# Performance work log

Hardware: AMD Instinct MI355X
Metric: run time of the kernel (lower is better)

The kernel has to match this reference:

```python
import jax, jax.numpy as jnp
import numpy as np

GRID = (32, 32, 32)  # must match init grid_size


def setup_inputs() -> dict:
    key = jax.random.key(0)
    # Mimic the module's init: D = 0.01 everywhere + 0.1 on the 6x6 diagonal,
    # plus small uniform noise so the baseline exercises non-degenerate values.
    D = jax.random.uniform(key, (6, 6, *GRID), dtype=jnp.float32) * 0.02 + 0.01
    D = D.at[jnp.arange(6), jnp.arange(6)].add(0.1)
    return {"D": D, "sx": 1, "sy": 1, "sz": 1, "ex": 30, "ey": 30, "ez": 30,
            "max_iterations": 300}


def reference(D, sx, sy, sz, ex, ey, ez, max_iterations):
    """flash_wave (training path, inference=False): 300-step CA as one lax.scan.

    Returns the stacked history of phi (pre-update, as the torch loop appends
    phi at the top of each iteration): shape [max_iterations, 6, X, Y, Z].
    Early exit is emulated by freezing phi once the wave reaches (ex,ey,ez),
    so no per-step host sync is needed.
    """
    phi0 = jnp.zeros((6, *GRID), dtype=D.dtype).at[:, sx, sy, sz].set(1.0)
    active_D = D + 0.95  # inference=False branch

    def body(carry, _):
        phi, done = carry
        # 6x6 channel mixing per grid cell: 'oixyz,ixyz->oxyz'
        phi_out = jnp.einsum('oixyz,ixyz->oxyz', active_D, phi)
        pn = jnp.zeros_like(phi)
        pn = pn.at[0, 1:, :, :].set(phi_out[0, :-1, :, :])   # +x
        pn = pn.at[1, :-1, :, :].set(phi_out[1, 1:, :, :])   # -x
        pn = pn.at[2, :, 1:, :].set(phi_out[2, :, :-1, :])   # +y
        pn = pn.at[3, :, :-1, :].set(phi_out[3, :, 1:, :])   # -y
        pn = pn.at[4, :, :, 1:].set(phi_out[4, :, :, :-1])   # +z
        pn = pn.at[5, :, :, :-1].set(phi_out[5, :, :, 1:])   # -z
        nxt = jnp.clip(pn, 0.0, 1.0)
        nxt = jnp.where(done, phi, nxt)  # freeze after target reached
        reached = jnp.sum(nxt[:, ex, ey, ez]) > 0.01
        return (nxt, jnp.logical_or(done, reached)), phi

    (_, _), history = jax.lax.scan(body, (phi0, jnp.array(False)), None,
                                   length=int(max_iterations))
    return history
```

## Files before the change

kernel.cpp:

```cpp
#include <hip/hip_runtime.h>

#define NCH 6
#define NX 32
#define PLANE 1024
#define NCELL (NX * PLANE)
#define STEP_STRIDE (NCH * NCELL)
#define NTHREADS 256
#define NBLOCKS 128
#define RB 2

#define RING_WORDS ((size_t)RB * 3 * NCELL)
#define F_DONE 0

typedef unsigned long long u64;

__device__ __forceinline__ u64 ld64(const u64* p) {
    return __hip_atomic_load(p, __ATOMIC_RELAXED, __HIP_MEMORY_SCOPE_SYSTEM);
}
__device__ __forceinline__ void st64(u64* p, u64 v) {
    __hip_atomic_store(p, v, __ATOMIC_RELAXED, __HIP_MEMORY_SCOPE_SYSTEM);
}
__device__ __forceinline__ int ldi(const int* p) {
    return __hip_atomic_load(p, __ATOMIC_RELAXED, __HIP_MEMORY_SCOPE_SYSTEM);
}
__device__ __forceinline__ void sti(int* p, int v) {
    __hip_atomic_store(p, v, __ATOMIC_RELAXED, __HIP_MEMORY_SCOPE_SYSTEM);
}
__device__ __forceinline__ u64 pack2p(float a, float b, unsigned P) {
    const u64 w = ((u64)__float_as_uint(b) << 32) | __float_as_uint(a);
    return P ? (w | 0x8000000080000000ULL) : w;
}
__device__ __forceinline__ bool tagok(u64 w, unsigned P) {
    return (((unsigned)(w >> 63)) == P) & ((((unsigned)w) >> 31) == P);
}
__device__ __forceinline__ void unpack2(u64 w, float* d0, float* d1) {
    *d0 = __uint_as_float((unsigned)w & 0x7fffffffu);
    *d1 = __uint_as_float((unsigned)(w >> 32) & 0x7fffffffu);
}

__global__ void __launch_bounds__(NTHREADS)
BEMNA_V7_2_PhaseSpace_44117904064519_kernel(
    const float* __restrict__ D,
    const int* __restrict__ sx_p, const int* __restrict__ sy_p,
    const int* __restrict__ sz_p, const int* __restrict__ ex_p,
    const int* __restrict__ ey_p, const int* __restrict__ ez_p,
    const int* __restrict__ maxit_p,
    float* __restrict__ out,
    u64* __restrict__ ring,
    int* __restrict__ flags)
{
    const int tid  = (int)threadIdx.x;
    const int cell = (int)blockIdx.x * NTHREADS + tid;
    const int lane = tid & 63;
    const int x = cell >> 10;
    const int y = (cell >> 5) & 31;
    const int z = cell & 31;

    const int sx = *sx_p, sy = *sy_p, sz = *sz_p;
    const int ex = *ex_p, ey = *ey_p, ez = *ez_p;
    const int maxit = *maxit_p;
    const bool is_seed   = (cell == ((sx << 10) | (sy << 5) | sz));
    const bool is_target = (cell == ((ex << 10) | (ey << 5) | ez));

    const int  nbg[NCH] = { cell - PLANE, cell + PLANE, cell - 32, cell + 32, cell - 1, cell + 1 };
    const bool ok[NCH]  = { x >= 1, x <= 30, y >= 1, y <= 30, z >= 1, z <= 30 };

    const int cxm = ok[0] ? cell - PLANE : cell;
    const int cxp = ok[1] ? cell + PLANE : cell;
    const bool hi = (lane >= 32);
    const int cye = hi ? (ok[3] ? cell + 32 : cell)
                       : (ok[2] ? cell - 32 : cell);

    float dreg[NCH][NCH];
#pragma unroll
    for (int o = 0; o < NCH; ++o)
#pragma unroll
        for (int i = 0; i < NCH; ++i)
            dreg[o][i] = ok[o] ? D[(size_t)(o * NCH + i) * NCELL + nbg[o]] + 0.95f : 0.0f;

    float myv[NCH];
    const float iv = is_seed ? 1.0f : 0.0f;
    {
        const u64 p = pack2p(iv, iv, 0);
        st64(&ring[0 * NCELL + cell], p);
        st64(&ring[1 * NCELL + cell], p);
        st64(&ring[2 * NCELL + cell], p);
        float* outp = out + cell;
#pragma unroll
        for (int o = 0; o < NCH; ++o) { myv[o] = iv; outp[o * NCELL] = iv; }
    }

    int tripped = 0;
    for (int t = 0; t <= maxit - 2; ++t) {
        const u64* r0 = ring + (size_t)(t & 1) * 3 * NCELL;
        const u64* r1 = r0 + NCELL;
        const u64* r2 = r1 + NCELL;
        const unsigned P = (unsigned)((t >> 1) & 1);

        u64 a0, a1, a2, b0, b1, b2, c0, c1, c2;
        int ab = 0;
        for (;;) {
            a0 = ld64(r0 + cxm); a1 = ld64(r1 + cxm); a2 = ld64(r2 + cxm);
            b0 = ld64(r0 + cxp); b1 = ld64(r1 + cxp); b2 = ld64(r2 + cxp);
            c0 = ld64(r0 + cye); c1 = ld64(r1 + cye); c2 = ld64(r2 + cye);
            int dn = -1;
            if (lane == 0) dn = ldi(&flags[F_DONE]);
            dn = __shfl(dn, 0);
            const bool okr = tagok(a0, P) & tagok(a1, P) & tagok(a2, P)
                           & tagok(b0, P) & tagok(b1, P) & tagok(b2, P)
                           & tagok(c0, P) & tagok(c1, P) & tagok(c2, P);
            if (dn >= 0 && t + 1 > dn) { ab = 1; break; }
            if (__ballot(okr) == ~0ull) break;
            __builtin_amdgcn_s_sleep(1);
        }
        if (ab) break;

        float xm[NCH], xp[NCH], ye[NCH];
        unpack2(a0, &xm[0], &xm[1]); unpack2(a1, &xm[2], &xm[3]); unpack2(a2, &xm[4], &xm[5]);
        unpack2(b0, &xp[0], &xp[1]); unpack2(b1, &xp[2], &xp[3]); unpack2(b2, &xp[4], &xp[5]);
        unpack2(c0, &ye[0], &ye[1]); unpack2(c1, &ye[2], &ye[3]); unpack2(c2, &ye[4], &ye[5]);

        float ym[NCH], yp[NCH], zm[NCH], zp[NCH];
#pragma unroll
        for (int i = 0; i < NCH; ++i) {
            const float yin = __shfl(myv[i], lane ^ 32);
            zm[i] = __shfl(myv[i], (lane - 1) & 63);
            zp[i] = __shfl(myv[i], (lane + 1) & 63);
            ym[i] = hi ? yin : ye[i];
            yp[i] = hi ? ye[i] : yin;
        }

        float v[NCH];
        {
            float s0 = 0.f, s1 = 0.f, s2 = 0.f, s3 = 0.f, s4 = 0.f, s5 = 0.f;
#pragma unroll
            for (int i = 0; i < NCH; ++i) {
                s0 = fmaf(dreg[0][i], xm[i], s0);
                s1 = fmaf(dreg[1][i], xp[i], s1);
                s2 = fmaf(dreg[2][i], ym[i], s2);
                s3 = fmaf(dreg[3][i], yp[i], s3);
                s4 = fmaf(dreg[4][i], zm[i], s4);
                s5 = fmaf(dreg[5][i], zp[i], s5);
            }
            v[0] = fminf(fmaxf(s0, 0.f), 1.f);
            v[1] = fminf(fmaxf(s1, 0.f), 1.f);
            v[2] = fminf(fmaxf(s2, 0.f), 1.f);
            v[3] = fminf(fmaxf(s3, 0.f), 1.f);
            v[4] = fminf(fmaxf(s4, 0.f), 1.f);
            v[5] = fminf(fmaxf(s5, 0.f), 1.f);
        }

        if (is_target && !tripped) {
            if (v[0] + v[1] + v[2] + v[3] + v[4] + v[5] > 0.01f) {
                sti(&flags[F_DONE], t + 1);
                tripped = 1;
            }
        }

        {
            const unsigned P1 = (unsigned)(((t + 1) >> 1) & 1);
            u64* w0 = ring + (size_t)((t + 1) & 1) * 3 * NCELL;
            st64(w0 + 0 * NCELL + cell, pack2p(v[0], v[1], P1));
            st64(w0 + 1 * NCELL + cell, pack2p(v[2], v[3], P1));
            st64(w0 + 2 * NCELL + cell, pack2p(v[4], v[5], P1));
        }

        {
            float* outp = out + (size_t)(t + 1) * STEP_STRIDE + cell;
#pragma unroll
            for (int o = 0; o < NCH; ++o) outp[o * NCELL] = v[o];
        }
#pragma unroll
        for (int o = 0; o < NCH; ++o) myv[o] = v[o];
    }
}

__global__ void fill_kernel(const int* __restrict__ flags,
                            float4* __restrict__ out,
                            int total4)
{
    const int s4 = STEP_STRIDE / 4;
    const int maxit = total4 / s4;
    const int ds = flags[F_DONE];
    const int tf = (ds >= 1 && ds <= maxit - 1) ? ds : maxit - 1;
    const int idx = (int)blockIdx.x * (int)blockDim.x + (int)threadIdx.x;
    const float4 v = out[(size_t)tf * s4 + idx];
    for (int t = tf + 1; t < maxit; ++t)
        out[(size_t)t * s4 + idx] = v;
}

extern "C" void kernel_launch(void* const* d_in, const int* in_sizes, int n_in,
                              void* d_out, int out_size, void* d_ws, size_t ws_size,
                              hipStream_t stream)
{
    const float* D   = (const float*)d_in[0];
    const int* sx    = (const int*)d_in[1];
    const int* sy    = (const int*)d_in[2];
    const int* sz    = (const int*)d_in[3];
    const int* ex    = (const int*)d_in[4];
    const int* ey    = (const int*)d_in[5];
    const int* ez    = (const int*)d_in[6];
    const int* maxit = (const int*)d_in[7];
    float* out = (float*)d_out;

    u64* ring  = (u64*)d_ws;
    int* flags = (int*)(ring + RING_WORDS);

    BEMNA_V7_2_PhaseSpace_44117904064519_kernel<<<dim3(NBLOCKS), dim3(NTHREADS), 0, stream>>>(
        D, sx, sy, sz, ex, ey, ez, maxit, out, ring, flags);

    const int total4 = out_size / 4;
    fill_kernel<<<dim3((STEP_STRIDE / 4) / 256), dim3(256), 0, stream>>>(
        flags, (float4*)out, total4);
}
```

Before: 406.6 us.

## Fuse two CA steps per grid sync using halo-expanded LDS tiles

Each block now owns a 1x8x32 slab and loads a halo-extended 3x12x32 tile from the global ring into shared memory. It computes an intermediate step over a 3x10 region redundantly, then the owned step from it. This halves the number of cross-block global ring handshakes per simulated step, which is the dominant latency, in exchange for redundant compute, larger blocks of 1024 threads and more LDS traffic. The fill kernel also gains a second grid dimension so the tail copy of the frozen state is split across more blocks.

```diff
diff --git a/kernel.cpp b/kernel.cpp
--- a/kernel.cpp
+++ b/kernel.cpp
@@ -5,9 +5,11 @@
 #define PLANE 1024
 #define NCELL (NX * PLANE)
 #define STEP_STRIDE (NCH * NCELL)
-#define NTHREADS 256
+#define NTHREADS 1024
 #define NBLOCKS 128
 #define RB 2
+#define NE 960
+#define NT3 1152
 
 #define RING_WORDS ((size_t)RB * 3 * NCELL)
 #define F_DONE 0
@@ -38,7 +40,7 @@
     *d1 = __uint_as_float((unsigned)(w >> 32) & 0x7fffffffu);
 }
 
-__global__ void __launch_bounds__(NTHREADS)
+__global__ void __launch_bounds__(NTHREADS, 1)
 BEMNA_V7_2_PhaseSpace_44117904064519_kernel(
     const float* __restrict__ D,
     const int* __restrict__ sx_p, const int* __restrict__ sy_p,
@@ -49,129 +51,202 @@
     u64* __restrict__ ring,
     int* __restrict__ flags)
 {
-    const int tid  = (int)threadIdx.x;
-    const int cell = (int)blockIdx.x * NTHREADS + tid;
-    const int lane = tid & 63;
-    const int x = cell >> 10;
-    const int y = (cell >> 5) & 31;
-    const int z = cell & 31;
+    __shared__ float Tb[NCH][NT3];
+    __shared__ float Eb[NCH][NE];
+    __shared__ int lds_dn;
+    volatile int* vdn = &lds_dn;
+
+    const int tid = (int)threadIdx.x;
+    const int bx  = (int)blockIdx.x;
+    const int x   = bx >> 2;
+    const int ys  = (bx & 3) << 3;
 
     const int sx = *sx_p, sy = *sy_p, sz = *sz_p;
-    const int ex = *ex_p, ey = *ey_p, ez = *ez_p;
+    const int ex = *ex_p, ey = *ey_p, ez_ = *ez_p;
     const int maxit = *maxit_p;
-    const bool is_seed   = (cell == ((sx << 10) | (sy << 5) | sz));
-    const bool is_target = (cell == ((ex << 10) | (ey << 5) | ez));
-
-    const int  nbg[NCH] = { cell - PLANE, cell + PLANE, cell - 32, cell + 32, cell - 1, cell + 1 };
-    const bool ok[NCH]  = { x >= 1, x <= 30, y >= 1, y <= 30, z >= 1, z <= 30 };
-
-    const int cxm = ok[0] ? cell - PLANE : cell;
-    const int cxp = ok[1] ? cell + PLANE : cell;
-    const bool hi = (lane >= 32);
-    const int cye = hi ? (ok[3] ? cell + 32 : cell)
-                       : (ok[2] ? cell - 32 : cell);
-
+    const int seedc = (sx << 10) | (sy << 5) | sz;
+    const int targc = (ex << 10) | (ey << 5) | ez_;
+
+    const int anchor = (x << 10) + (ys << 5) + (tid & 31);
+
+    int cTA = anchor, slA = 0; bool inA = false;
+    if (tid < NT3) {
+        const int dp = tid / 384, rem = tid - dp * 384;
+        const int r2 = rem >> 5, zz = rem & 31;
+        const int gx = x - 1 + dp, gy = ys - 2 + r2;
+        slA = tid;
+        if (gx >= 0 && gx < 32 && gy >= 0 && gy < 32) { inA = true; cTA = (gx << 10) + (gy << 5) + zz; }
+    }
+    int cTB = anchor, slB = 0; bool inB = false;
+    if (tid < NT3 - 1024) {
+        const int slot = tid + 1024;
+        const int dp = slot / 384, rem = slot - dp * 384;
+        const int r2 = rem >> 5, zz = rem & 31;
+        const int gx = x - 1 + dp, gy = ys - 2 + r2;
+        slB = slot;
+        if (gx >= 0 && gx < 32 && gy >= 0 && gy < 32) { inB = true; cTB = (gx << 10) + (gy << 5) + zz; }
+    }
+
+    const bool eact = (tid < NE);
+    int dx = 0, ry = 0, ez = tid & 31, xe = x, ye = ys;
+    bool ein = false;
+    int celle = anchor;
+    if (eact) {
+        dx = tid / 320; const int rem = tid - dx * 320; ry = rem >> 5; ez = rem & 31;
+        xe = x - 1 + dx; ye = ys - 1 + ry;
+        ein = (xe >= 0 && xe < 32 && ye >= 0 && ye < 32);
+        if (ein) celle = (xe << 10) + (ye << 5) + ez;
+    }
+    const bool own = ein && (dx == 1) && (ry >= 1) && (ry <= 8);
+    const bool is_seed   = own && (celle == seedc);
+    const bool is_target = own && (celle == targc);
+
+    int cP = anchor;
+    if (eact && ein && dx == 0 && x - 2 >= 0)  cP = ((x - 2) << 10) + (ye << 5) + ez;
+    if (eact && ein && dx == 2 && x + 2 <= 31) cP = ((x + 2) << 10) + (ye << 5) + ez;
+
+    const int  nbg[NCH] = { celle - PLANE, celle + PLANE, celle - 32, celle + 32, celle - 1, celle + 1 };
+    const bool okn[NCH] = { ein && xe >= 1, ein && xe <= 30, ein && ye >= 1,
+                            ein && ye <= 30, ein && ez >= 1, ein && ez <= 30 };
     float dreg[NCH][NCH];
 #pragma unroll
     for (int o = 0; o < NCH; ++o)
 #pragma unroll
         for (int i = 0; i < NCH; ++i)
-            dreg[o][i] = ok[o] ? D[(size_t)(o * NCH + i) * NCELL + nbg[o]] + 0.95f : 0.0f;
-
-    float myv[NCH];
-    const float iv = is_seed ? 1.0f : 0.0f;
-    {
+            dreg[o][i] = okn[o] ? D[(size_t)(o * NCH + i) * NCELL + nbg[o]] + 0.95f : 0.0f;
+
+    const int ts3  = (dx * 12 + ry + 1) * 32 + ez;
+    const int tpa0 = (ts3 - 384 >= 0) ? ts3 - 384 : 0;
+    const int tpa1 = (ts3 + 384 < NT3) ? ts3 + 384 : NT3 - 1;
+    const int tp2 = ts3 - 32, tp3 = ts3 + 32;
+    const int tp4 = (ez >= 1) ? ts3 - 1 : ts3, tp5 = (ez <= 30) ? ts3 + 1 : ts3;
+    const int en0 = tid - 320, en1 = tid + 320, en2 = tid - 32, en3 = tid + 32;
+    const int en4 = (ez >= 1) ? tid - 1 : tid, en5 = (ez <= 30) ? tid + 1 : tid;
+
+    for (int k = tid; k < NCH * NT3; k += NTHREADS) ((float*)Tb)[k] = 0.0f;
+    for (int k = tid; k < NCH * NE;  k += NTHREADS) ((float*)Eb)[k] = 0.0f;
+    if (tid == 0) lds_dn = -1;
+    if (own) {
+        const float iv = is_seed ? 1.0f : 0.0f;
         const u64 p = pack2p(iv, iv, 0);
-        st64(&ring[0 * NCELL + cell], p);
-        st64(&ring[1 * NCELL + cell], p);
-        st64(&ring[2 * NCELL + cell], p);
-        float* outp = out + cell;
-#pragma unroll
-        for (int o = 0; o < NCH; ++o) { myv[o] = iv; outp[o * NCELL] = iv; }
-    }
+        st64(&ring[0 * NCELL + celle], p);
+        st64(&ring[1 * NCELL + celle], p);
+        st64(&ring[2 * NCELL + celle], p);
+#pragma unroll
+        for (int o = 0; o < NCH; ++o) out[o * NCELL + celle] = iv;
+    }
+    __syncthreads();
 
     int tripped = 0;
-    for (int t = 0; t <= maxit - 2; ++t) {
-        const u64* r0 = ring + (size_t)(t & 1) * 3 * NCELL;
+    for (int ss = 0; 2 * ss + 1 <= maxit - 1; ++ss) {
+        const u64* r0 = ring + (size_t)(ss & 1) * 3 * NCELL;
         const u64* r1 = r0 + NCELL;
         const u64* r2 = r1 + NCELL;
-        const unsigned P = (unsigned)((t >> 1) & 1);
-
-        u64 a0, a1, a2, b0, b1, b2, c0, c1, c2;
-        int ab = 0;
+        const unsigned P = (unsigned)((ss >> 1) & 1);
+
+        u64 a0, a1, a2, b0, b1, b2, p0, p1, p2;
         for (;;) {
-            a0 = ld64(r0 + cxm); a1 = ld64(r1 + cxm); a2 = ld64(r2 + cxm);
-            b0 = ld64(r0 + cxp); b1 = ld64(r1 + cxp); b2 = ld64(r2 + cxp);
-            c0 = ld64(r0 + cye); c1 = ld64(r1 + cye); c2 = ld64(r2 + cye);
-            int dn = -1;
-            if (lane == 0) dn = ldi(&flags[F_DONE]);
-            dn = __shfl(dn, 0);
+            a0 = ld64(r0 + cTA); a1 = ld64(r1 + cTA); a2 = ld64(r2 + cTA);
+            b0 = ld64(r0 + cTB); b1 = ld64(r1 + cTB); b2 = ld64(r2 + cTB);
+            p0 = ld64(r0 + cP);  p1 = ld64(r1 + cP);  p2 = ld64(r2 + cP);
+            int dnv = -1;
+            if ((tid & 63) == 0) dnv = ldi(&flags[F_DONE]);
+            if (dnv >= 0) *vdn = dnv;
             const bool okr = tagok(a0, P) & tagok(a1, P) & tagok(a2, P)
                            & tagok(b0, P) & tagok(b1, P) & tagok(b2, P)
-                           & tagok(c0, P) & tagok(c1, P) & tagok(c2, P);
-            if (dn >= 0 && t + 1 > dn) { ab = 1; break; }
+                           & tagok(p0, P) & tagok(p1, P) & tagok(p2, P);
+            const int d = *vdn;
+            if (d >= 0 && 2 * ss + 1 > d) break;
             if (__ballot(okr) == ~0ull) break;
             __builtin_amdgcn_s_sleep(1);
         }
-        if (ab) break;
-
-        float xm[NCH], xp[NCH], ye[NCH];
-        unpack2(a0, &xm[0], &xm[1]); unpack2(a1, &xm[2], &xm[3]); unpack2(a2, &xm[4], &xm[5]);
-        unpack2(b0, &xp[0], &xp[1]); unpack2(b1, &xp[2], &xp[3]); unpack2(b2, &xp[4], &xp[5]);
-        unpack2(c0, &ye[0], &ye[1]); unpack2(c1, &ye[2], &ye[3]); unpack2(c2, &ye[4], &ye[5]);
-
-        float ym[NCH], yp[NCH], zm[NCH], zp[NCH];
-#pragma unroll
-        for (int i = 0; i < NCH; ++i) {
-            const float yin = __shfl(myv[i], lane ^ 32);
-            zm[i] = __shfl(myv[i], (lane - 1) & 63);
-            zp[i] = __shfl(myv[i], (lane + 1) & 63);
-            ym[i] = hi ? yin : ye[i];
-            yp[i] = hi ? ye[i] : yin;
-        }
-
-        float v[NCH];
-        {
+        if (inA) {
+            unpack2(a0, &Tb[0][slA], &Tb[1][slA]);
+            unpack2(a1, &Tb[2][slA], &Tb[3][slA]);
+            unpack2(a2, &Tb[4][slA], &Tb[5][slA]);
+        }
+        if (inB) {
+            unpack2(b0, &Tb[0][slB], &Tb[1][slB]);
+            unpack2(b1, &Tb[2][slB], &Tb[3][slB]);
+            unpack2(b2, &Tb[4][slB], &Tb[5][slB]);
+        }
+        float pX[NCH];
+        unpack2(p0, &pX[0], &pX[1]); unpack2(p1, &pX[2], &pX[3]); unpack2(p2, &pX[4], &pX[5]);
+
+        __syncthreads();
+        { const int d = *vdn; if (d >= 0 && 2 * ss + 1 > d) break; }
+
+        float v1[NCH] = {0, 0, 0, 0, 0, 0};
+        if (eact) {
             float s0 = 0.f, s1 = 0.f, s2 = 0.f, s3 = 0.f, s4 = 0.f, s5 = 0.f;
 #pragma unroll
             for (int i = 0; i < NCH; ++i) {
-                s0 = fmaf(dreg[0][i], xm[i], s0);
-                s1 = fmaf(dreg[1][i], xp[i], s1);
-                s2 = fmaf(dreg[2][i], ym[i], s2);
-                s3 = fmaf(dreg[3][i], yp[i], s3);
-                s4 = fmaf(dreg[4][i], zm[i], s4);
-                s5 = fmaf(dreg[5][i], zp[i], s5);
-            }
-            v[0] = fminf(fmaxf(s0, 0.f), 1.f);
-            v[1] = fminf(fmaxf(s1, 0.f), 1.f);
-            v[2] = fminf(fmaxf(s2, 0.f), 1.f);
-            v[3] = fminf(fmaxf(s3, 0.f), 1.f);
-            v[4] = fminf(fmaxf(s4, 0.f), 1.f);
-            v[5] = fminf(fmaxf(s5, 0.f), 1.f);
-        }
-
-        if (is_target && !tripped) {
-            if (v[0] + v[1] + v[2] + v[3] + v[4] + v[5] > 0.01f) {
-                sti(&flags[F_DONE], t + 1);
+                const float xi0 = (dx == 0) ? pX[i] : Tb[i][tpa0];
+                const float xi1 = (dx == 2) ? pX[i] : Tb[i][tpa1];
+                s0 = fmaf(dreg[0][i], xi0, s0);
+                s1 = fmaf(dreg[1][i], xi1, s1);
+                s2 = fmaf(dreg[2][i], Tb[i][tp2], s2);
+                s3 = fmaf(dreg[3][i], Tb[i][tp3], s3);
+                s4 = fmaf(dreg[4][i], Tb[i][tp4], s4);
+                s5 = fmaf(dreg[5][i], Tb[i][tp5], s5);
+            }
+            v1[0] = fminf(fmaxf(s0, 0.f), 1.f);
+            v1[1] = fminf(fmaxf(s1, 0.f), 1.f);
+            v1[2] = fminf(fmaxf(s2, 0.f), 1.f);
+            v1[3] = fminf(fmaxf(s3, 0.f), 1.f);
+            v1[4] = fminf(fmaxf(s4, 0.f), 1.f);
+            v1[5] = fminf(fmaxf(s5, 0.f), 1.f);
+        }
+        if (own) {
+            float* op = out + (size_t)(2 * ss + 1) * STEP_STRIDE + celle;
+#pragma unroll
+            for (int o = 0; o < NCH; ++o) op[o * NCELL] = v1[o];
+            if (is_target && !tripped &&
+                (v1[0] + v1[1] + v1[2] + v1[3] + v1[4] + v1[5] > 0.01f)) {
+                sti(&flags[F_DONE], 2 * ss + 1);
                 tripped = 1;
             }
         }
-
-        {
-            const unsigned P1 = (unsigned)(((t + 1) >> 1) & 1);
-            u64* w0 = ring + (size_t)((t + 1) & 1) * 3 * NCELL;
-            st64(w0 + 0 * NCELL + cell, pack2p(v[0], v[1], P1));
-            st64(w0 + 1 * NCELL + cell, pack2p(v[2], v[3], P1));
-            st64(w0 + 2 * NCELL + cell, pack2p(v[4], v[5], P1));
-        }
-
-        {
-            float* outp = out + (size_t)(t + 1) * STEP_STRIDE + cell;
-#pragma unroll
-            for (int o = 0; o < NCH; ++o) outp[o * NCELL] = v[o];
-        }
-#pragma unroll
-        for (int o = 0; o < NCH; ++o) myv[o] = v[o];
+        if (eact) {
+#pragma unroll
+            for (int i = 0; i < NCH; ++i) Eb[i][tid] = v1[i];
+        }
+        __syncthreads();
+
+        if (own) {
+            float s0 = 0.f, s1 = 0.f, s2 = 0.f, s3 = 0.f, s4 = 0.f, s5 = 0.f;
+#pragma unroll
+            for (int i = 0; i < NCH; ++i) {
+                s0 = fmaf(dreg[0][i], Eb[i][en0], s0);
+                s1 = fmaf(dreg[1][i], Eb[i][en1], s1);
+                s2 = fmaf(dreg[2][i], Eb[i][en2], s2);
+                s3 = fmaf(dreg[3][i], Eb[i][en3], s3);
+                s4 = fmaf(dreg[4][i], Eb[i][en4], s4);
+                s5 = fmaf(dreg[5][i], Eb[i][en5], s5);
+            }
+            float v2[NCH];
+            v2[0] = fminf(fmaxf(s0, 0.f), 1.f);
+            v2[1] = fminf(fmaxf(s1, 0.f), 1.f);
+            v2[2] = fminf(fmaxf(s2, 0.f), 1.f);
+            v2[3] = fminf(fmaxf(s3, 0.f), 1.f);
+            v2[4] = fminf(fmaxf(s4, 0.f), 1.f);
+            v2[5] = fminf(fmaxf(s5, 0.f), 1.f);
+            if (is_target && !tripped &&
+                (v2[0] + v2[1] + v2[2] + v2[3] + v2[4] + v2[5] > 0.01f)) {
+                sti(&flags[F_DONE], 2 * ss + 2);
+                tripped = 1;
+            }
+            const unsigned P1 = (unsigned)(((ss + 1) >> 1) & 1);
+            u64* w = ring + (size_t)((ss + 1) & 1) * 3 * NCELL;
+            st64(w + 0 * NCELL + celle, pack2p(v2[0], v2[1], P1));
+            st64(w + 1 * NCELL + celle, pack2p(v2[2], v2[3], P1));
+            st64(w + 2 * NCELL + celle, pack2p(v2[4], v2[5], P1));
+            if (2 * ss + 2 <= maxit - 1) {
+                float* op = out + (size_t)(2 * ss + 2) * STEP_STRIDE + celle;
+#pragma unroll
+                for (int o = 0; o < NCH; ++o) op[o * NCELL] = v2[o];
+            }
+        }
     }
 }
 
@@ -185,7 +260,7 @@
     const int tf = (ds >= 1 && ds <= maxit - 1) ? ds : maxit - 1;
     const int idx = (int)blockIdx.x * (int)blockDim.x + (int)threadIdx.x;
     const float4 v = out[(size_t)tf * s4 + idx];
-    for (int t = tf + 1; t < maxit; ++t)
+    for (int t = tf + 1 + (int)blockIdx.y; t < maxit; t += (int)gridDim.y)
         out[(size_t)t * s4 + idx] = v;
 }
 
@@ -210,6 +285,6 @@
         D, sx, sy, sz, ex, ey, ez, maxit, out, ring, flags);
 
     const int total4 = out_size / 4;
-    fill_kernel<<<dim3((STEP_STRIDE / 4) / 256), dim3(256), 0, stream>>>(
+    fill_kernel<<<dim3((STEP_STRIDE / 4) / 256, 8), dim3(256), 0, stream>>>(
         flags, (float4*)out, total4);
 }
```

New measurement: 445.1 us. +9.5%, slower.

## Tile blocks as 2x8x32 slabs with LDS halo exchange and neighbor-progress sync

Applied to the files above, without the earlier changes.

Each block now covers a 2(x) by 8(y) by 32(z) slab of cells. Neighbor values inside the block are exchanged through shared memory, so only true halo cells are polled from the global ring. Halo reads are skipped while the wavefront cannot yet have reached them, based on Manhattan distance from the seed. The ring grows to 8 slots with 2-bit tags, and blocks enforce a bounded lead over their neighbors through per-block progress flags. The fill kernel also gets a second grid dimension so the time steps after early exit are written in parallel. The aim is less global polling traffic and lower per-step sync latency, at the cost of per-step __syncthreads and more complex flag logic.

```diff
diff --git a/kernel.cpp b/kernel.cpp
--- a/kernel.cpp
+++ b/kernel.cpp
@@ -5,12 +5,14 @@
 #define PLANE 1024
 #define NCELL (NX * PLANE)
 #define STEP_STRIDE (NCH * NCELL)
-#define NTHREADS 256
-#define NBLOCKS 128
-#define RB 2
+#define NTHREADS 512
+#define NBLOCKS 64
+#define RB 8
+#define MLEAD 6
 
 #define RING_WORDS ((size_t)RB * 3 * NCELL)
 #define F_DONE 0
+#define F_PROG 16
 
 typedef unsigned long long u64;
 
@@ -26,12 +28,18 @@
 __device__ __forceinline__ void sti(int* p, int v) {
     __hip_atomic_store(p, v, __ATOMIC_RELAXED, __HIP_MEMORY_SCOPE_SYSTEM);
 }
-__device__ __forceinline__ u64 pack2p(float a, float b, unsigned P) {
-    const u64 w = ((u64)__float_as_uint(b) << 32) | __float_as_uint(a);
-    return P ? (w | 0x8000000080000000ULL) : w;
-}
-__device__ __forceinline__ bool tagok(u64 w, unsigned P) {
-    return (((unsigned)(w >> 63)) == P) & ((((unsigned)w) >> 31) == P);
+__device__ __forceinline__ u64 pack2(float a, float b) {
+    return ((u64)__float_as_uint(b) << 32) | __float_as_uint(a);
+}
+__device__ __forceinline__ u64 pack2t(float a, float b, unsigned tg) {
+    u64 w = pack2(a, b);
+    if (tg & 1u) w |= 0x80000000ULL;
+    if (tg & 2u) w |= 0x8000000000000000ULL;
+    return w;
+}
+__device__ __forceinline__ bool tagchk(u64 w, unsigned tg) {
+    return ((((unsigned)(w >> 31)) & 1u) == (tg & 1u)) &
+           ((((unsigned)(w >> 63)) & 1u) == (tg >> 1));
 }
 __device__ __forceinline__ void unpack2(u64 w, float* d0, float* d1) {
     *d0 = __uint_as_float((unsigned)w & 0x7fffffffu);
@@ -49,12 +57,21 @@
     u64* __restrict__ ring,
     int* __restrict__ flags)
 {
+    __shared__ u64 Tb[2][3][NTHREADS];
+    __shared__ int lds_dn;
+    volatile int* vdn = &lds_dn;
+
     const int tid  = (int)threadIdx.x;
-    const int cell = (int)blockIdx.x * NTHREADS + tid;
+    const int bx   = (int)blockIdx.x;
+    const int cx   = bx >> 2;
+    const int st   = bx & 3;
+    const int lx   = tid >> 8;
+    const int row  = (tid >> 5) & 7;
+    const int z    = tid & 31;
     const int lane = tid & 63;
-    const int x = cell >> 10;
-    const int y = (cell >> 5) & 31;
-    const int z = cell & 31;
+    const int gx   = (cx << 1) + lx;
+    const int gy   = (st << 3) + row;
+    const int cell = (gx << 10) + (gy << 5) + z;
 
     const int sx = *sx_p, sy = *sy_p, sz = *sz_p;
     const int ex = *ex_p, ey = *ey_p, ez = *ez_p;
@@ -62,85 +79,112 @@
     const bool is_seed   = (cell == ((sx << 10) | (sy << 5) | sz));
     const bool is_target = (cell == ((ex << 10) | (ey << 5) | ez));
 
+    const bool has_x = lx ? (gx <= 30) : (gx >= 1);
+    const int  gxh   = lx ? gx + 1 : gx - 1;
+    const int  cellx = has_x ? ((gxh << 10) + (gy << 5) + z) : cell;
+    const int  distx = abs(gxh - sx) + abs(gy - sy) + abs(z - sz);
+    const bool has_y = (row == 0) ? (gy >= 1) : ((row == 7) ? (gy <= 30) : false);
+    const int  gyh   = (row == 0) ? gy - 1 : gy + 1;
+    const int  celly = has_y ? ((gx << 10) + (gyh << 5) + z) : cell;
+    const int  disty = abs(gx - sx) + abs(gyh - sy) + abs(z - sz);
+
+    const int xin = lx ? tid - 256 : tid + 256;
+    const int yin = ((row & 1) ? tid + 32 : tid - 32) & (NTHREADS - 1);
+
     const int  nbg[NCH] = { cell - PLANE, cell + PLANE, cell - 32, cell + 32, cell - 1, cell + 1 };
-    const bool ok[NCH]  = { x >= 1, x <= 30, y >= 1, y <= 30, z >= 1, z <= 30 };
-
-    const int cxm = ok[0] ? cell - PLANE : cell;
-    const int cxp = ok[1] ? cell + PLANE : cell;
-    const bool hi = (lane >= 32);
-    const int cye = hi ? (ok[3] ? cell + 32 : cell)
-                       : (ok[2] ? cell - 32 : cell);
-
+    const bool okn[NCH] = { gx >= 1, gx <= 30, gy >= 1, gy <= 30, z >= 1, z <= 30 };
     float dreg[NCH][NCH];
 #pragma unroll
     for (int o = 0; o < NCH; ++o)
 #pragma unroll
         for (int i = 0; i < NCH; ++i)
-            dreg[o][i] = ok[o] ? D[(size_t)(o * NCH + i) * NCELL + nbg[o]] + 0.95f : 0.0f;
+            dreg[o][i] = okn[o] ? D[(size_t)(o * NCH + i) * NCELL + nbg[o]] + 0.95f : 0.0f;
 
     float myv[NCH];
     const float iv = is_seed ? 1.0f : 0.0f;
     {
-        const u64 p = pack2p(iv, iv, 0);
+        const u64 p = pack2(iv, iv);
         st64(&ring[0 * NCELL + cell], p);
         st64(&ring[1 * NCELL + cell], p);
         st64(&ring[2 * NCELL + cell], p);
-        float* outp = out + cell;
-#pragma unroll
-        for (int o = 0; o < NCH; ++o) { myv[o] = iv; outp[o * NCELL] = iv; }
+        Tb[0][0][tid] = p; Tb[0][1][tid] = p; Tb[0][2][tid] = p;
+#pragma unroll
+        for (int o = 0; o < NCH; ++o) { myv[o] = iv; out[o * NCELL + cell] = iv; }
     }
-
-    int tripped = 0;
+    if (tid == 0) { lds_dn = -1; sti(&flags[F_PROG + bx * 16], 0); }
+    __syncthreads();
+
+    int tripped = 0, lastmin = 0;
     for (int t = 0; t <= maxit - 2; ++t) {
-        const u64* r0 = ring + (size_t)(t & 1) * 3 * NCELL;
-        const u64* r1 = r0 + NCELL;
-        const u64* r2 = r1 + NCELL;
-        const unsigned P = (unsigned)((t >> 1) & 1);
-
-        u64 a0, a1, a2, b0, b1, b2, c0, c1, c2;
-        int ab = 0;
-        for (;;) {
-            a0 = ld64(r0 + cxm); a1 = ld64(r1 + cxm); a2 = ld64(r2 + cxm);
-            b0 = ld64(r0 + cxp); b1 = ld64(r1 + cxp); b2 = ld64(r2 + cxp);
-            c0 = ld64(r0 + cye); c1 = ld64(r1 + cye); c2 = ld64(r2 + cye);
-            int dn = -1;
-            if (lane == 0) dn = ldi(&flags[F_DONE]);
-            dn = __shfl(dn, 0);
-            const bool okr = tagok(a0, P) & tagok(a1, P) & tagok(a2, P)
-                           & tagok(b0, P) & tagok(b1, P) & tagok(b2, P)
-                           & tagok(c0, P) & tagok(c1, P) & tagok(c2, P);
-            if (dn >= 0 && t + 1 > dn) { ab = 1; break; }
-            if (__ballot(okr) == ~0ull) break;
-            __builtin_amdgcn_s_sleep(1);
-        }
-        if (ab) break;
-
-        float xm[NCH], xp[NCH], ye[NCH];
-        unpack2(a0, &xm[0], &xm[1]); unpack2(a1, &xm[2], &xm[3]); unpack2(a2, &xm[4], &xm[5]);
-        unpack2(b0, &xp[0], &xp[1]); unpack2(b1, &xp[2], &xp[3]); unpack2(b2, &xp[4], &xp[5]);
-        unpack2(c0, &ye[0], &ye[1]); unpack2(c1, &ye[2], &ye[3]); unpack2(c2, &ye[4], &ye[5]);
-
-        float ym[NCH], yp[NCH], zm[NCH], zp[NCH];
-#pragma unroll
-        for (int i = 0; i < NCH; ++i) {
-            const float yin = __shfl(myv[i], lane ^ 32);
-            zm[i] = __shfl(myv[i], (lane - 1) & 63);
-            zp[i] = __shfl(myv[i], (lane + 1) & 63);
-            ym[i] = hi ? yin : ye[i];
-            yp[i] = hi ? ye[i] : yin;
-        }
-
+        const u64* rs = ring + (size_t)(t & (RB - 1)) * 3 * NCELL;
+        const unsigned tg = (unsigned)((t >> 2) & 3);
+
+        const bool needx = has_x && (t >= distx);
+        const bool needy = has_y && (t >= disty);
+        float rx[NCH] = {0,0,0,0,0,0}, ry[NCH] = {0,0,0,0,0,0};
+        if (__ballot(needx || needy) != 0ull) {
+            u64 hx0 = 0, hx1 = 0, hx2 = 0, hy0 = 0, hy1 = 0, hy2 = 0;
+            for (;;) {
+                if (needx) { hx0 = ld64(rs + cellx); hx1 = ld64(rs + NCELL + cellx); hx2 = ld64(rs + 2 * NCELL + cellx); }
+                if (needy) { hy0 = ld64(rs + celly); hy1 = ld64(rs + NCELL + celly); hy2 = ld64(rs + 2 * NCELL + celly); }
+                if (lane == 0) { const int dnv = ldi(&flags[F_DONE]); if (dnv >= 0) *vdn = dnv; }
+                bool okr = true;
+                if (needx) okr = okr & tagchk(hx0, tg) & tagchk(hx1, tg) & tagchk(hx2, tg);
+                if (needy) okr = okr & tagchk(hy0, tg) & tagchk(hy1, tg) & tagchk(hy2, tg);
+                const int d = *vdn;
+                if (d >= 0 && t + 1 > d) break;
+                if (__ballot(okr) == ~0ull) break;
+                __builtin_amdgcn_s_sleep(1);
+            }
+            if (needx) { unpack2(hx0, &rx[0], &rx[1]); unpack2(hx1, &rx[2], &rx[3]); unpack2(hx2, &rx[4], &rx[5]); }
+            if (needy) { unpack2(hy0, &ry[0], &ry[1]); unpack2(hy1, &ry[2], &ry[3]); unpack2(hy2, &ry[4], &ry[5]); }
+        } else if (((t & 3) == 0) && lane == 0) {
+            const int dnv = ldi(&flags[F_DONE]); if (dnv >= 0) *vdn = dnv;
+        }
+
+        if (tid == 0 && (t + 1 - lastmin > MLEAD)) {
+            for (;;) {
+                int mn = 0x7fffffff;
+                if (cx > 0)  mn = min(mn, ldi(&flags[F_PROG + (bx - 4) * 16]));
+                if (cx < 15) mn = min(mn, ldi(&flags[F_PROG + (bx + 4) * 16]));
+                if (st > 0)  mn = min(mn, ldi(&flags[F_PROG + (bx - 1) * 16]));
+                if (st < 3)  mn = min(mn, ldi(&flags[F_PROG + (bx + 1) * 16]));
+                const int dnv = ldi(&flags[F_DONE]); if (dnv >= 0) *vdn = dnv;
+                const int d = *vdn;
+                if (d >= 0 && t + 1 > d) break;
+                if (mn >= t + 1 - MLEAD) { lastmin = mn; break; }
+                __builtin_amdgcn_s_sleep(2);
+            }
+        }
+        __syncthreads();
+        { const int d = *vdn; if (d >= 0 && t + 1 > d) break; }
+
+        float LX[NCH], LY[NCH];
+        {
+            const u64 q0 = Tb[t & 1][0][xin], q1 = Tb[t & 1][1][xin], q2 = Tb[t & 1][2][xin];
+            unpack2(q0, &LX[0], &LX[1]); unpack2(q1, &LX[2], &LX[3]); unpack2(q2, &LX[4], &LX[5]);
+            const u64 p0 = Tb[t & 1][0][yin], p1 = Tb[t & 1][1][yin], p2 = Tb[t & 1][2][yin];
+            unpack2(p0, &LY[0], &LY[1]); unpack2(p1, &LY[2], &LY[3]); unpack2(p2, &LY[4], &LY[5]);
+        }
+        const bool odd = (row & 1) != 0;
         float v[NCH];
         {
             float s0 = 0.f, s1 = 0.f, s2 = 0.f, s3 = 0.f, s4 = 0.f, s5 = 0.f;
 #pragma unroll
             for (int i = 0; i < NCH; ++i) {
-                s0 = fmaf(dreg[0][i], xm[i], s0);
-                s1 = fmaf(dreg[1][i], xp[i], s1);
-                s2 = fmaf(dreg[2][i], ym[i], s2);
-                s3 = fmaf(dreg[3][i], yp[i], s3);
-                s4 = fmaf(dreg[4][i], zm[i], s4);
-                s5 = fmaf(dreg[5][i], zp[i], s5);
+                const float pairv = __shfl(myv[i], lane ^ 32);
+                const float zmv   = __shfl(myv[i], (lane + 63) & 63);
+                const float zpv   = __shfl(myv[i], (lane + 1) & 63);
+                const float xmv = lx ? LX[i] : rx[i];
+                const float xpv = lx ? rx[i] : LX[i];
+                const float ymv = odd ? pairv : (row > 0 ? LY[i] : ry[i]);
+                const float ypv = odd ? (row < 7 ? LY[i] : ry[i]) : pairv;
+                s0 = fmaf(dreg[0][i], xmv, s0);
+                s1 = fmaf(dreg[1][i], xpv, s1);
+                s2 = fmaf(dreg[2][i], ymv, s2);
+                s3 = fmaf(dreg[3][i], ypv, s3);
+                s4 = fmaf(dreg[4][i], zmv, s4);
+                s5 = fmaf(dreg[5][i], zpv, s5);
             }
             v[0] = fminf(fmaxf(s0, 0.f), 1.f);
             v[1] = fminf(fmaxf(s1, 0.f), 1.f);
@@ -150,26 +194,27 @@
             v[5] = fminf(fmaxf(s5, 0.f), 1.f);
         }
 
-        if (is_target && !tripped) {
-            if (v[0] + v[1] + v[2] + v[3] + v[4] + v[5] > 0.01f) {
-                sti(&flags[F_DONE], t + 1);
-                tripped = 1;
-            }
+        if (is_target && !tripped &&
+            (v[0] + v[1] + v[2] + v[3] + v[4] + v[5] > 0.01f)) {
+            sti(&flags[F_DONE], t + 1);
+            tripped = 1;
         }
 
         {
-            const unsigned P1 = (unsigned)(((t + 1) >> 1) & 1);
-            u64* w0 = ring + (size_t)((t + 1) & 1) * 3 * NCELL;
-            st64(w0 + 0 * NCELL + cell, pack2p(v[0], v[1], P1));
-            st64(w0 + 1 * NCELL + cell, pack2p(v[2], v[3], P1));
-            st64(w0 + 2 * NCELL + cell, pack2p(v[4], v[5], P1));
-        }
-
-        {
-            float* outp = out + (size_t)(t + 1) * STEP_STRIDE + cell;
-#pragma unroll
-            for (int o = 0; o < NCH; ++o) outp[o * NCELL] = v[o];
-        }
+            const unsigned tg1 = (unsigned)(((t + 1) >> 2) & 3);
+            u64* wsl = ring + (size_t)((t + 1) & (RB - 1)) * 3 * NCELL;
+            st64(wsl + cell,             pack2t(v[0], v[1], tg1));
+            st64(wsl + NCELL + cell,     pack2t(v[2], v[3], tg1));
+            st64(wsl + 2 * NCELL + cell, pack2t(v[4], v[5], tg1));
+            Tb[(t + 1) & 1][0][tid] = pack2(v[0], v[1]);
+            Tb[(t + 1) & 1][1][tid] = pack2(v[2], v[3]);
+            Tb[(t + 1) & 1][2][tid] = pack2(v[4], v[5]);
+            float* op = out + (size_t)(t + 1) * STEP_STRIDE + cell;
+#pragma unroll
+            for (int o = 0; o < NCH; ++o) op[o * NCELL] = v[o];
+        }
+        if (tid == 0) sti(&flags[F_PROG + bx * 16], t + 1);
+        __syncthreads();
 #pragma unroll
         for (int o = 0; o < NCH; ++o) myv[o] = v[o];
     }
@@ -185,7 +230,7 @@
     const int tf = (ds >= 1 && ds <= maxit - 1) ? ds : maxit - 1;
     const int idx = (int)blockIdx.x * (int)blockDim.x + (int)threadIdx.x;
     const float4 v = out[(size_t)tf * s4 + idx];
-    for (int t = tf + 1; t < maxit; ++t)
+    for (int t = tf + 1 + (int)blockIdx.y; t < maxit; t += (int)gridDim.y)
         out[(size_t)t * s4 + idx] = v;
 }
 
@@ -210,6 +255,6 @@
         D, sx, sy, sz, ex, ey, ez, maxit, out, ring, flags);
 
     const int total4 = out_size / 4;
-    fill_kernel<<<dim3((STEP_STRIDE / 4) / 256), dim3(256), 0, stream>>>(
+    fill_kernel<<<dim3((STEP_STRIDE / 4) / 256, 8), dim3(256), 0, stream>>>(
         flags, (float4*)out, total4);
 }
```

Result: slower. 454.2 us (+11.7%).
